# Optimization experiments

Measured on AMD Instinct MI355X. Metric: run time of the kernel, lower is better.

## Reference

```python
import jax, jax.numpy as jnp
import numpy as np
from functools import partial

K = 10
ALPHA = 0.1
N_NODES = 100000
N_EDGES = 1600000
IN_C, HID_C, OUT_C = 512, 256, 64


def setup_inputs() -> dict:
    key = jax.random.key(0)
    k1, k2, k3, k4, k5 = jax.random.split(key, 5)
    x = jax.random.normal(k1, (N_NODES, IN_C), dtype=jnp.float32)
    edge_index = jax.random.randint(k2, (2, N_EDGES), 0, N_NODES, dtype=jnp.int64)
    # Linear params (torch Linear: y = x @ W.T + b), Kaiming-ish scale
    w1 = jax.random.normal(k3, (HID_C, IN_C), dtype=jnp.float32) / np.sqrt(IN_C)
    b1 = jnp.zeros((HID_C,), dtype=jnp.float32)
    w2 = jax.random.normal(k4, (OUT_C, HID_C), dtype=jnp.float32) / np.sqrt(HID_C)
    b2 = jnp.zeros((OUT_C,), dtype=jnp.float32)
    return {"x": x, "edge_index": edge_index, "w1": w1, "b1": b1, "w2": w2, "b2": b2}


def _gcn_norm(edge_index, num_nodes):
    # add self-loops, symmetric normalization: norm_e = d[src]^-1/2 * d[dst]^-1/2
    loops = jnp.arange(num_nodes, dtype=edge_index.dtype)
    src = jnp.concatenate([edge_index[0], loops])
    dst = jnp.concatenate([edge_index[1], loops])
    ones = jnp.ones_like(dst, dtype=jnp.float32)
    deg = jax.ops.segment_sum(ones, dst, num_segments=num_nodes)
    dinv = jnp.where(deg > 0, jax.lax.rsqrt(deg), 0.0)
    norm = dinv[src] * dinv[dst]
    return src, dst, norm


def reference(x, edge_index, w1, b1, w2, b2):
    # inference mode: dropout = identity
    h = jax.nn.relu(x @ w1.T + b1)
    h = h @ w2.T + b2  # [N, OUT_C]
    n = x.shape[0]
    src, dst, norm = _gcn_norm(edge_index, n)
    h0 = h

    def step(hcur, _):
        msg = hcur[src] * norm[:, None]                      # gather [E+N, C]
        agg = jax.ops.segment_sum(msg, dst, num_segments=n)  # scatter-add [N, C]
        return (1.0 - ALPHA) * agg + ALPHA * h0, None

    h, _ = jax.lax.scan(step, h, None, length=K)
    return h
```

## Files before the change

kernel.cpp:

```cpp
#include <hip/hip_runtime.h>
#include <hip/hip_bf16.h>

#define N_NODES 100000
#define N_EDGES 1600000
#define IN_C 512
#define HID_C 256
#define OUT_C 64
#define K_ITERS 10
#define ALPHA 0.1f

typedef float f32x4 __attribute__((ext_vector_type(4)));
typedef _Float16 f16;
typedef _Float16 f16x4 __attribute__((ext_vector_type(4)));
typedef _Float16 f16x8 __attribute__((ext_vector_type(8)));

#define MFMA16(a, b, c) __builtin_amdgcn_mfma_f32_16x16x32_f16((a), (b), (c), 0, 0, 0)

__device__ __forceinline__ void gload16(const void* g, void* l) {
    __builtin_amdgcn_global_load_lds(
        (const __attribute__((address_space(1))) unsigned int*)g,
        (__attribute__((address_space(3))) unsigned int*)l, 16, 0, 0);
}

__global__ void k_count(const int* __restrict__ ei, int* __restrict__ cnt, int E) {
    int e = blockIdx.x * blockDim.x + threadIdx.x;
    if (e < E) atomicAdd(&cnt[ei[E + e]], 1);
}

__global__ void k_dinv(const int* __restrict__ cnt, float* __restrict__ dinv, int n) {
    int i = blockIdx.x * blockDim.x + threadIdx.x;
    if (i < n) dinv[i] = rsqrtf((float)cnt[i] + 1.0f);
}

#define SCB 1024
__global__ __launch_bounds__(256) void k_scan1(const int* __restrict__ cnt,
                                               int* __restrict__ bsum, int n) {
    __shared__ int s[256];
    int b = blockIdx.x, t = threadIdx.x;
    int base = b * SCB + t * 4;
    int local = 0;
#pragma unroll
    for (int j = 0; j < 4; ++j) {
        int i = base + j;
        if (i < n) local += cnt[i];
    }
    s[t] = local;
    __syncthreads();
    for (int off = 1; off < 256; off <<= 1) {
        int u = (t >= off) ? s[t - off] : 0;
        __syncthreads();
        s[t] += u;
        __syncthreads();
    }
    if (t == 255) bsum[b] = s[255];
}

__global__ __launch_bounds__(128) void k_scan2(const int* __restrict__ bsum,
                                               int* __restrict__ boff, int G,
                                               int* __restrict__ row_ptr, int n, int total) {
    __shared__ int s[128];
    int t = threadIdx.x;
    int v = (t < G) ? bsum[t] : 0;
    s[t] = v;
    __syncthreads();
    for (int off = 1; off < 128; off <<= 1) {
        int u = (t >= off) ? s[t - off] : 0;
        __syncthreads();
        s[t] += u;
        __syncthreads();
    }
    if (t < G) boff[t] = s[t] - v;
    if (t == 0) row_ptr[n] = total;
}

__global__ __launch_bounds__(256) void k_scan3(const int* __restrict__ cnt,
                                               const int* __restrict__ boff,
                                               int* __restrict__ row_ptr,
                                               int* __restrict__ cursor, int n) {
    __shared__ int s[256];
    int b = blockIdx.x, t = threadIdx.x;
    int base = b * SCB + t * 4;
    int c4[4];
    int local = 0;
#pragma unroll
    for (int j = 0; j < 4; ++j) {
        int i = base + j;
        c4[j] = (i < n) ? cnt[i] : 0;
        local += c4[j];
    }
    s[t] = local;
    __syncthreads();
    for (int off = 1; off < 256; off <<= 1) {
        int u = (t >= off) ? s[t - off] : 0;
        __syncthreads();
        s[t] += u;
        __syncthreads();
    }
    int run = boff[b] + s[t] - local;
#pragma unroll
    for (int j = 0; j < 4; ++j) {
        int i = base + j;
        if (i < n) {
            row_ptr[i] = run;
            cursor[i] = run;
            run += c4[j];
        }
    }
}

__global__ void k_fill(const int* __restrict__ ei, const float* __restrict__ dinv,
                       int* __restrict__ cursor, int2* __restrict__ csr_pack, int E) {
    int e = blockIdx.x * blockDim.x + threadIdx.x;
    if (e < E) {
        int s = ei[e];
        int d = ei[E + e];
        int pos = atomicAdd(&cursor[d], 1);
        csr_pack[pos] = make_int2(s, __float_as_int(dinv[s] * dinv[d]));
    }
}

__global__ void k_cast(const float* __restrict__ in, f16* __restrict__ out, int n) {
    int i = blockIdx.x * blockDim.x + threadIdx.x;
    if (i < n) out[i] = (f16)in[i];
}

__global__ __launch_bounds__(512, 4) void k_mlp2(
    const float* __restrict__ x,
    const f16* __restrict__ w1h,
    const float* __restrict__ b1,
    const f16* __restrict__ w2h,
    const float* __restrict__ b2,
    f16* __restrict__ h016, f16* __restrict__ hcur16, int n) {
    __shared__ __align__(16) union {
        struct {
            f16 Ah[2][128 * 40];
            f16 Bh[2][256 * 32];
        } p1;
        struct {
            f16 Hh[128 * 264];
        } p2;
    } sm;

    const int tid = threadIdx.x;
    const int l = tid & 63;
    const int w = tid >> 6;
    const int wr = w >> 2;
    const int wc = w & 3;
    const int lr = l & 15;
    const int kg = l >> 4;
    const int row0 = blockIdx.x * 128;

    const int r0 = tid >> 3, kk0 = (tid & 7) * 4;
    int gr0 = row0 + r0;       if (gr0 >= n) gr0 = n - 1;
    int gr1 = row0 + r0 + 64;  if (gr1 >= n) gr1 = n - 1;
    const float* xp0 = &x[(size_t)gr0 * IN_C + kk0];
    const float* xp1 = &x[(size_t)gr1 * IN_C + kk0];

    int brow[2], bkc[2], bsb[2];
#pragma unroll
    for (int i = 0; i < 2; ++i) {
        int slot = tid + 512 * i;
        brow[i] = slot >> 2;
        bkc[i] = (slot & 3) ^ ((brow[i] >> 1) & 3);
        bsb[i] = (w * 64 + 512 * i) * 8;
    }

    f32x4 acc[4][4];
#pragma unroll
    for (int m = 0; m < 4; ++m)
#pragma unroll
        for (int nf = 0; nf < 4; ++nf) acc[m][nf] = (f32x4)0.0f;

    {
        float4 v0 = *(const float4*)xp0;
        float4 v1 = *(const float4*)xp1;
#pragma unroll
        for (int i = 0; i < 2; ++i)
            gload16(w1h + (size_t)brow[i] * IN_C + bkc[i] * 8, &sm.p1.Bh[0][bsb[i]]);
        f16x4 h4;
        h4.x = (f16)v0.x; h4.y = (f16)v0.y; h4.z = (f16)v0.z; h4.w = (f16)v0.w;
        *(f16x4*)&sm.p1.Ah[0][r0 * 40 + kk0] = h4;
        h4.x = (f16)v1.x; h4.y = (f16)v1.y; h4.z = (f16)v1.z; h4.w = (f16)v1.w;
        *(f16x4*)&sm.p1.Ah[0][(r0 + 64) * 40 + kk0] = h4;
    }
    __syncthreads();

    for (int ks = 0; ks < 16; ++ks) {
        const int cur = ks & 1;
        float4 xv0, xv1;
        if (ks < 15) {
            const int kn = (ks + 1) * 32;
            xv0 = *(const float4*)(xp0 + kn);
            xv1 = *(const float4*)(xp1 + kn);
#pragma unroll
            for (int i = 0; i < 2; ++i)
                gload16(w1h + (size_t)brow[i] * IN_C + kn + bkc[i] * 8,
                        &sm.p1.Bh[cur ^ 1][bsb[i]]);
        }

        f16x8 ah[4], bh[4];
#pragma unroll
        for (int m = 0; m < 4; ++m)
            ah[m] = *(const f16x8*)&sm.p1.Ah[cur][(wr * 64 + m * 16 + lr) * 40 + kg * 8];
#pragma unroll
        for (int nf = 0; nf < 4; ++nf) {
            int row = wc * 64 + nf * 16 + lr;
            int kc = kg ^ ((row >> 1) & 3);
            bh[nf] = *(const f16x8*)&sm.p1.Bh[cur][row * 32 + kc * 8];
        }
#pragma unroll
        for (int m = 0; m < 4; ++m)
#pragma unroll
            for (int nf = 0; nf < 4; ++nf)
                acc[m][nf] = MFMA16(ah[m], bh[nf], acc[m][nf]);

        if (ks < 15) {
            f16x4 h4;
            h4.x = (f16)xv0.x; h4.y = (f16)xv0.y; h4.z = (f16)xv0.z; h4.w = (f16)xv0.w;
            *(f16x4*)&sm.p1.Ah[cur ^ 1][r0 * 40 + kk0] = h4;
            h4.x = (f16)xv1.x; h4.y = (f16)xv1.y; h4.z = (f16)xv1.z; h4.w = (f16)xv1.w;
            *(f16x4*)&sm.p1.Ah[cur ^ 1][(r0 + 64) * 40 + kk0] = h4;
        }
        __syncthreads();
    }

#pragma unroll
    for (int m = 0; m < 4; ++m)
#pragma unroll
        for (int nf = 0; nf < 4; ++nf) {
            int col = wc * 64 + nf * 16 + lr;
            float bb = b1[col];
#pragma unroll
            for (int r = 0; r < 4; ++r) {
                int row = wr * 64 + m * 16 + kg * 4 + r;
                float hv = acc[m][nf][r] + bb;
                hv = fmaxf(hv, 0.0f);
                sm.p2.Hh[row * 264 + col] = (f16)hv;
            }
        }
    __syncthreads();

    f32x4 acc2[4];
#pragma unroll
    for (int m = 0; m < 4; ++m) acc2[m] = (f32x4)0.0f;
    const int col2 = wc * 16 + lr;
    const int rbase = wr * 64;

#pragma unroll
    for (int k0 = 0; k0 < HID_C; k0 += 32) {
        f16x8 b2h = *(const f16x8*)&w2h[(size_t)col2 * HID_C + k0 + kg * 8];
#pragma unroll
        for (int m = 0; m < 4; ++m) {
            f16x8 a2h = *(const f16x8*)&sm.p2.Hh[(rbase + m * 16 + lr) * 264 + k0 + kg * 8];
            acc2[m] = MFMA16(a2h, b2h, acc2[m]);
        }
    }

    float bb2 = b2[col2];
#pragma unroll
    for (int m = 0; m < 4; ++m)
#pragma unroll
        for (int r = 0; r < 4; ++r) {
            int grow = row0 + rbase + m * 16 + kg * 4 + r;
            if (grow < n) {
                float vv = acc2[m][r] + bb2;
                size_t idx = (size_t)grow * OUT_C + col2;
                h016[idx] = (f16)vv;
                hcur16[idx] = (f16)vv;
            }
        }
}

__global__ __launch_bounds__(256) void k_prop16(const f16* __restrict__ hin,
                                                const f16* __restrict__ h016,
                                                f16* __restrict__ hout,
                                                float* __restrict__ dout,
                                                const int* __restrict__ row_ptr,
                                                const int2* __restrict__ csr_pack,
                                                const float* __restrict__ dinv,
                                                int n, int final_iter) {
    const int gwave = (blockIdx.x * blockDim.x + threadIdx.x) >> 6;
    const int lane = threadIdx.x & 63;
    const int g = lane >> 3;
    const int cl = lane & 7;

    int node_raw = gwave * 8 + g;
    bool node_valid = node_raw < n;
    int node = node_valid ? node_raw : (n - 1);

    int e0 = row_ptr[node], e1 = row_ptr[node + 1];
    int nb = (e1 - e0 + 7) >> 3;
    nb = max(nb, __shfl_xor(nb, 8));
    nb = max(nb, __shfl_xor(nb, 16));
    nb = max(nb, __shfl_xor(nb, 32));

    float a[8];
#pragma unroll
    for (int q = 0; q < 8; ++q) a[q] = 0.0f;
    const int gbase = g * 8;

    int2 meta = csr_pack[min(e0 + cl, N_EDGES - 1)];
    for (int b = 0; b < nb; ++b) {
        int mbase = e0 + b * 8;
        int2 meta_next = meta;
        if (b + 1 < nb) meta_next = csr_pack[min(mbase + 8 + cl, N_EDGES - 1)];
#pragma unroll
        for (int j = 0; j < 8; ++j) {
            int s = __shfl(meta.x, gbase + j);
            float wv = __int_as_float(__shfl(meta.y, gbase + j));
            if (mbase + j < e1) {
                f16x8 v = *(const f16x8*)&hin[(size_t)s * OUT_C + cl * 8];
#pragma unroll
                for (int q = 0; q < 8; ++q) a[q] += wv * (float)v[q];
            }
        }
        meta = meta_next;
    }

    float dv = dinv[node];
    float d2 = dv * dv;
    size_t idx = (size_t)node * OUT_C + cl * 8;
    f16x8 sv = *(const f16x8*)&hin[idx];
    f16x8 h0v = *(const f16x8*)&h016[idx];
    float r[8];
#pragma unroll
    for (int q = 0; q < 8; ++q)
        r[q] = (1.0f - ALPHA) * (a[q] + d2 * (float)sv[q]) + ALPHA * (float)h0v[q];

    if (node_valid) {
        f16x8 o;
#pragma unroll
        for (int q = 0; q < 8; ++q) o[q] = (f16)r[q];
        *(f16x8*)&hout[idx] = o;
        if (final_iter) {
            float4 o0 = make_float4(r[0], r[1], r[2], r[3]);
            float4 o1 = make_float4(r[4], r[5], r[6], r[7]);
            *(float4*)&dout[idx] = o0;
            *(float4*)&dout[idx + 4] = o1;
        }
    }
}

extern "C" void kernel_launch(void* const* d_in, const int* in_sizes, int n_in,
                              void* d_out, int out_size, void* d_ws, size_t ws_size,
                              hipStream_t stream) {
    const float* x  = (const float*)d_in[0];
    const int*   ei = (const int*)d_in[1];
    const float* w1 = (const float*)d_in[2];
    const float* b1 = (const float*)d_in[3];
    const float* w2 = (const float*)d_in[4];
    const float* b2 = (const float*)d_in[5];
    float* dout = (float*)d_out;

    const int N = N_NODES;
    const int E = N_EDGES;
    const int G = (N + SCB - 1) / SCB;

    f16*   h16A    = (f16*)d_ws;
    f16*   h16B    = h16A + (size_t)N * OUT_C;
    f16*   h016    = h16B + (size_t)N * OUT_C;
    int2*  csr_pack = (int2*)(h016 + (size_t)N * OUT_C);
    float* dinv    = (float*)(csr_pack + E);
    int*   cnt     = (int*)(dinv + N);
    int*   row_ptr = cnt + N;
    int*   cursor  = row_ptr + (N + 1);
    f16*   w1h     = (f16*)(cursor + N);
    f16*   w2h     = w1h + (size_t)HID_C * IN_C;
    int*   bsum    = (int*)(w2h + (size_t)OUT_C * HID_C);
    int*   boff    = bsum + 128;

    hipMemsetAsync(cnt, 0, (size_t)N * sizeof(int), stream);

    k_count<<<(E + 255) / 256, 256, 0, stream>>>(ei, cnt, E);
    k_dinv<<<(N + 255) / 256, 256, 0, stream>>>(cnt, dinv, N);
    k_scan1<<<G, 256, 0, stream>>>(cnt, bsum, N);
    k_scan2<<<1, 128, 0, stream>>>(bsum, boff, G, row_ptr, N, E);
    k_scan3<<<G, 256, 0, stream>>>(cnt, boff, row_ptr, cursor, N);
    k_fill<<<(E + 255) / 256, 256, 0, stream>>>(ei, dinv, cursor, csr_pack, E);

    k_cast<<<(HID_C * IN_C + 255) / 256, 256, 0, stream>>>(w1, w1h, HID_C * IN_C);
    k_cast<<<(OUT_C * HID_C + 255) / 256, 256, 0, stream>>>(w2, w2h, OUT_C * HID_C);

    k_mlp2<<<(N + 127) / 128, 512, 0, stream>>>(x, w1h, b1, w2h, b2, h016, h16A, N);

    const int pwaves = (N + 7) / 8;
    const int pblocks = (pwaves * 64 + 255) / 256;
    for (int it = 0; it < K_ITERS; ++it) {
        const f16* pin = (it & 1) ? h16B : h16A;
        f16* pout = (it & 1) ? h16A : h16B;
        k_prop16<<<pblocks, 256, 0, stream>>>(pin, h016, pout, dout, row_ptr,
                                              csr_pack, dinv, N,
                                              it == K_ITERS - 1 ? 1 : 0);
    }
}
```

Before: 603.5 us.

## Split node features into four column chunks for cache-local propagation

Stores the fp16 feature matrices as four 16-column planes, each a contiguous [N,16] array, instead of row-major [N,64]. The propagation grid now covers chunk x node-block, with each block reading only one plane. Each gathered row slice shrinks to 32 bytes and the working set per plane is a quarter of the full matrix, aimed at better L2/MALL hit rates for the random gathers. The cost is that the CSR metadata is re-read four times and each load is narrower (8 bytes per lane), so there are more memory instructions per byte.

```diff
diff --git a/kernel.cpp b/kernel.cpp
--- a/kernel.cpp
+++ b/kernel.cpp
@@ -8,6 +8,7 @@
 #define OUT_C 64
 #define K_ITERS 10
 #define ALPHA 0.1f
+#define NCHUNK 4
 
 typedef float f32x4 __attribute__((ext_vector_type(4)));
 typedef _Float16 f16;
@@ -257,6 +258,7 @@
     }
 
     float bb2 = b2[col2];
+    const size_t cbase = (size_t)wc * N_NODES * 16;
 #pragma unroll
     for (int m = 0; m < 4; ++m)
 #pragma unroll
@@ -264,7 +266,7 @@
             int grow = row0 + rbase + m * 16 + kg * 4 + r;
             if (grow < n) {
                 float vv = acc2[m][r] + bb2;
-                size_t idx = (size_t)grow * OUT_C + col2;
+                size_t idx = cbase + (size_t)grow * 16 + lr;
                 h016[idx] = (f16)vv;
                 hcur16[idx] = (f16)vv;
             }
@@ -279,39 +281,46 @@
                                                 const int2* __restrict__ csr_pack,
                                                 const float* __restrict__ dinv,
                                                 int n, int final_iter) {
-    const int gwave = (blockIdx.x * blockDim.x + threadIdx.x) >> 6;
+    const int chunk = blockIdx.x & 3;
+    const int nbidx = blockIdx.x >> 2;
     const int lane = threadIdx.x & 63;
-    const int g = lane >> 3;
-    const int cl = lane & 7;
-
-    int node_raw = gwave * 8 + g;
+    const int wv = threadIdx.x >> 6;
+    const int g = lane >> 2;
+    const int cl = lane & 3;
+
+    int node_raw = nbidx * 64 + wv * 16 + g;
     bool node_valid = node_raw < n;
     int node = node_valid ? node_raw : (n - 1);
 
+    const f16* hin_c = hin + (size_t)chunk * N_NODES * 16;
+    const f16* h0_c = h016 + (size_t)chunk * N_NODES * 16;
+    f16* hout_c = hout + (size_t)chunk * N_NODES * 16;
+
     int e0 = row_ptr[node], e1 = row_ptr[node + 1];
-    int nb = (e1 - e0 + 7) >> 3;
+    int nb = (e1 - e0 + 3) >> 2;
+    nb = max(nb, __shfl_xor(nb, 4));
     nb = max(nb, __shfl_xor(nb, 8));
     nb = max(nb, __shfl_xor(nb, 16));
     nb = max(nb, __shfl_xor(nb, 32));
 
-    float a[8];
-#pragma unroll
-    for (int q = 0; q < 8; ++q) a[q] = 0.0f;
-    const int gbase = g * 8;
+    float a[4];
+#pragma unroll
+    for (int q = 0; q < 4; ++q) a[q] = 0.0f;
+    const int gbase = g * 4;
 
     int2 meta = csr_pack[min(e0 + cl, N_EDGES - 1)];
     for (int b = 0; b < nb; ++b) {
-        int mbase = e0 + b * 8;
+        int mbase = e0 + b * 4;
         int2 meta_next = meta;
-        if (b + 1 < nb) meta_next = csr_pack[min(mbase + 8 + cl, N_EDGES - 1)];
-#pragma unroll
-        for (int j = 0; j < 8; ++j) {
+        if (b + 1 < nb) meta_next = csr_pack[min(mbase + 4 + cl, N_EDGES - 1)];
+#pragma unroll
+        for (int j = 0; j < 4; ++j) {
             int s = __shfl(meta.x, gbase + j);
-            float wv = __int_as_float(__shfl(meta.y, gbase + j));
+            float wvv = __int_as_float(__shfl(meta.y, gbase + j));
             if (mbase + j < e1) {
-                f16x8 v = *(const f16x8*)&hin[(size_t)s * OUT_C + cl * 8];
-#pragma unroll
-                for (int q = 0; q < 8; ++q) a[q] += wv * (float)v[q];
+                f16x4 v = *(const f16x4*)&hin_c[(size_t)s * 16 + cl * 4];
+#pragma unroll
+                for (int q = 0; q < 4; ++q) a[q] += wvv * (float)v[q];
             }
         }
         meta = meta_next;
@@ -319,24 +328,22 @@
 
     float dv = dinv[node];
     float d2 = dv * dv;
-    size_t idx = (size_t)node * OUT_C + cl * 8;
-    f16x8 sv = *(const f16x8*)&hin[idx];
-    f16x8 h0v = *(const f16x8*)&h016[idx];
-    float r[8];
-#pragma unroll
-    for (int q = 0; q < 8; ++q)
+    size_t idx = (size_t)node * 16 + cl * 4;
+    f16x4 sv = *(const f16x4*)&hin_c[idx];
+    f16x4 h0v = *(const f16x4*)&h0_c[idx];
+    float r[4];
+#pragma unroll
+    for (int q = 0; q < 4; ++q)
         r[q] = (1.0f - ALPHA) * (a[q] + d2 * (float)sv[q]) + ALPHA * (float)h0v[q];
 
     if (node_valid) {
-        f16x8 o;
-#pragma unroll
-        for (int q = 0; q < 8; ++q) o[q] = (f16)r[q];
-        *(f16x8*)&hout[idx] = o;
+        f16x4 o;
+#pragma unroll
+        for (int q = 0; q < 4; ++q) o[q] = (f16)r[q];
+        *(f16x4*)&hout_c[idx] = o;
         if (final_iter) {
-            float4 o0 = make_float4(r[0], r[1], r[2], r[3]);
-            float4 o1 = make_float4(r[4], r[5], r[6], r[7]);
-            *(float4*)&dout[idx] = o0;
-            *(float4*)&dout[idx + 4] = o1;
+            float4 of = make_float4(r[0], r[1], r[2], r[3]);
+            *(float4*)&dout[(size_t)node * OUT_C + chunk * 16 + cl * 4] = of;
         }
     }
 }
@@ -383,13 +390,13 @@
 
     k_mlp2<<<(N + 127) / 128, 512, 0, stream>>>(x, w1h, b1, w2h, b2, h016, h16A, N);
 
-    const int pwaves = (N + 7) / 8;
-    const int pblocks = (pwaves * 64 + 255) / 256;
+    const int nodeblocks = (N + 63) / 64;
+    const int pgrid = nodeblocks * NCHUNK;
     for (int it = 0; it < K_ITERS; ++it) {
         const f16* pin = (it & 1) ? h16B : h16A;
         f16* pout = (it & 1) ? h16A : h16B;
-        k_prop16<<<pblocks, 256, 0, stream>>>(pin, h016, pout, dout, row_ptr,
-                                              csr_pack, dinv, N,
-                                              it == K_ITERS - 1 ? 1 : 0);
-    }
-}
+        k_prop16<<<pgrid, 256, 0, stream>>>(pin, h016, pout, dout, row_ptr,
+                                            csr_pack, dinv, N,
+                                            it == K_ITERS - 1 ? 1 : 0);
+    }
+}
```

After: 1.002 ms. 66.1% more time.
